# Kernel tuning notes

Hardware: AMD Instinct MI355X
Metric: run time of the kernel (lower is better)

The kernel has to match this reference:

```python
import jax, jax.numpy as jnp
import numpy as np
from jax import lax

B, C, H, W = 2, 128, 96, 96
K = 3
KK = K * K
EPS = 1e-5


def setup_inputs() -> dict:
    key = jax.random.key(0)
    ks = jax.random.split(key, 4)
    d = {"hu": jax.random.normal(ks[0], (B, C, H, W), jnp.float32)}
    for i in range(3):
        k = jax.random.split(ks[i + 1], 7)
        d["off_w%d" % (i + 1)] = jax.random.normal(k[0], (3 * KK, C, K, K), jnp.float32) * 0.01
        d["off_b%d" % (i + 1)] = jax.random.normal(k[1], (3 * KK,), jnp.float32) * 0.01
        d["w%d" % (i + 1)] = jax.random.normal(k[2], (C, C, K, K), jnp.float32) / np.float32(np.sqrt(C * KK))
        d["g%d" % (i + 1)] = jax.random.uniform(k[3], (C,), jnp.float32) + 0.5
        d["b%d" % (i + 1)] = jax.random.normal(k[4], (C,), jnp.float32) * 0.1
        d["m%d" % (i + 1)] = jax.random.normal(k[5], (C,), jnp.float32) * 0.1
        d["v%d" % (i + 1)] = jax.random.uniform(k[6], (C,), jnp.float32) + 0.5
    return d


def _mod_deform_conv(x, w, offset, mask, dilation):
    # x: [B,C,H,W]; offset: [B,2*KK,H,W] (dy,dx interleaved per kernel tap);
    # mask: [B,KK,H,W] (already sigmoid'ed). Zero padding outside the image.
    Hh, Ww = x.shape[2], x.shape[3]
    pad = dilation * (K - 1) // 2
    ky = jnp.repeat(jnp.arange(K), K).astype(x.dtype)  # [KK] row of each tap
    kx = jnp.tile(jnp.arange(K), K).astype(x.dtype)    # [KK] col of each tap
    gy = (jnp.arange(Hh, dtype=x.dtype) - pad)[None, :, None] + (ky * dilation)[:, None, None]  # [KK,H,1]
    gx = (jnp.arange(Ww, dtype=x.dtype) - pad)[None, None, :] + (kx * dilation)[:, None, None]  # [KK,1,W]
    off = offset.reshape(x.shape[0], KK, 2, Hh, Ww)
    py = gy[None] + off[:, :, 0]  # [B,KK,H,W] sampling row
    px = gx[None] + off[:, :, 1]  # [B,KK,H,W] sampling col

    def sample_one(xb, pyb, pxb, mb):
        # xb: [C,H,W]; pyb/pxb/mb: [KK,H,W]
        y0 = jnp.floor(pyb)
        x0 = jnp.floor(pxb)
        ly = pyb - y0
        lx = pxb - x0
        acc = jnp.zeros((xb.shape[0],) + pyb.shape, xb.dtype)
        for dy, wy in ((0, 1.0 - ly), (1, ly)):
            for dx, wx in ((0, 1.0 - lx), (1, lx)):
                yi = y0 + dy
                xi = x0 + dx
                valid = (yi >= 0) & (yi <= Hh - 1) & (xi >= 0) & (xi <= Ww - 1)
                yc = jnp.clip(yi, 0, Hh - 1).astype(jnp.int32)
                xc = jnp.clip(xi, 0, Ww - 1).astype(jnp.int32)
                v = xb[:, yc, xc]  # gather -> [C,KK,H,W]
                acc = acc + v * (wy * wx * valid.astype(xb.dtype))[None]
        return acc * mb[None]  # modulation

    sampled = jax.vmap(sample_one)(x, py, px, mask)  # [B,C,KK,H,W]
    return jnp.einsum('bckhw,ock->bohw', sampled, w.reshape(w.shape[0], w.shape[1], KK))


def _block(x, off_w, off_b, w, g, b, m, v, dilation):
    pad = dilation * (K - 1) // 2
    om = lax.conv_general_dilated(
        x, off_w, (1, 1), [(pad, pad), (pad, pad)],
        rhs_dilation=(dilation, dilation),
        dimension_numbers=('NCHW', 'OIHW', 'NCHW')) + off_b[None, :, None, None]
    offset = om[:, :2 * KK]
    mask = jax.nn.sigmoid(om[:, 2 * KK:])
    y = _mod_deform_conv(x, w, offset, mask, dilation)
    scale = (g / jnp.sqrt(v + EPS))[None, :, None, None]  # BN (inference form)
    y = (y - m[None, :, None, None]) * scale + b[None, :, None, None]
    return jax.nn.relu(y)


def reference(hu, off_w1, off_b1, w1, g1, b1, m1, v1,
              off_w2, off_b2, w2, g2, b2, m2, v2,
              off_w3, off_b3, w3, g3, b3, m3, v3):
    a1 = _block(hu, off_w1, off_b1, w1, g1, b1, m1, v1, 2) + hu
    a2 = _block(a1, off_w2, off_b2, w2, g2, b2, m2, v2, 4) + a1
    a3 = _block(a2, off_w3, off_b3, w3, g3, b3, m3, v3, 8) + a2
    return a3
```

## Files before the change

kernel.cpp:

```cpp
#include <hip/hip_runtime.h>
#include <math.h>

constexpr int Bn  = 2;
constexpr int Cn  = 128;
constexpr int Hn  = 96;
constexpr int Wn  = 96;
constexpr int HWn = Hn * Wn;
constexpr int CHWn = Cn * HWn;
constexpr int KCn = Cn * 9;
constexpr float EPSn = 1e-5f;
constexpr int KPAD = 1160;

typedef short bf16x8 __attribute__((ext_vector_type(8)));
typedef float f32x4  __attribute__((ext_vector_type(4)));

static __device__ inline short f2bf(float f) {
    union { float f; unsigned u; } v; v.f = f;
    unsigned r = v.u + 0x7fff + ((v.u >> 16) & 1);
    return (short)(r >> 16);
}
static __device__ inline unsigned pack2(float a, float b) {
    unsigned r;
    asm("v_cvt_pk_bf16_f32 %0, %1, %2" : "=v"(r) : "v"(a), "v"(b));
    return r;
}
static __device__ inline float bflo(unsigned u) { return __int_as_float(u << 16); }
static __device__ inline float bfhi(unsigned u) { return __int_as_float(u & 0xffff0000u); }

__global__ __launch_bounds__(256) void prep_all(
    const float* __restrict__ hu,
    const float* __restrict__ w1, const float* __restrict__ w2,
    const float* __restrict__ w3,
    const float* __restrict__ o1, const float* __restrict__ o2,
    const float* __restrict__ o3,
    short* __restrict__ wbs, short* __restrict__ owbs,
    unsigned short* __restrict__ xTb)
{
    __shared__ float Tl[128][65];
    const int bid = blockIdx.x;
    if (bid < 1728) {
        const int stage = bid / 576;
        const float* w = (stage == 0) ? w1 : (stage == 1) ? w2 : w3;
        int t = (bid - stage * 576) * 256 + threadIdx.x;
        int e = t & 7, l = (t >> 3) & 63, rest = t >> 9;
        int j = rest % 36, g = rest / 36;
        int lr = l & 15, lq = l >> 4;
        int o = g * 16 + lr;
        int kidx = j * 32 + lq * 8 + e;
        int k = kidx >> 7, c = kidx & 127;
        wbs[stage * Cn * KCn + t] = f2bf(w[o * KCn + c * 9 + k]);
    } else if (bid < 2160) {
        const int rb = bid - 1728;
        const int stage = rb / 144;
        const float* ow = (stage == 0) ? o1 : (stage == 1) ? o2 : o3;
        int t = (rb - stage * 144) * 256 + threadIdx.x;
        int e = t & 7, l = (t >> 3) & 63, rest = t >> 9;
        int kk = rest % 9, wvv = rest / 9;
        int mh = wvv & 1, ks = wvv >> 1;
        int lr = l & 15, lq = l >> 4;
        int o = mh * 16 + lr;
        int kidx = ks * 288 + kk * 32 + lq * 8 + e;
        int k = kidx >> 7, c = kidx & 127;
        owbs[stage * 32 * KCn + t] = (o < 27) ? f2bf(ow[o * KCn + c * 9 + k]) : (short)0;
    } else {
        const int t = threadIdx.x;
        const int pix0 = (bid - 2160) * 64;
        const int b   = pix0 / HWn;
        const int sp0 = pix0 - b * HWn;
        const float* xb = hu + b * CHWn + sp0 + (t & 63);
        const int c0 = t >> 6;
#pragma unroll 8
        for (int i = 0; i < 32; ++i) {
            const int c = c0 + 4 * i;
            Tl[c][t & 63] = xb[c * HWn];
        }
        __syncthreads();
        unsigned short* dstb = xTb + pix0 * 128;
#pragma unroll 8
        for (int i = 0; i < 32; ++i) {
            const int o = t + 256 * i;
            dstb[o] = (unsigned short)f2bf(Tl[o & 127][o >> 7]);
        }
    }
}

__global__ __launch_bounds__(512, 8) void fused_stage(
    const unsigned short* __restrict__ xTb,
    const short* __restrict__ wbs, const short* __restrict__ owbs,
    const float* __restrict__ obv,
    const float* __restrict__ gv, const float* __restrict__ bv,
    const float* __restrict__ mv, const float* __restrict__ vv,
    unsigned short* __restrict__ outTb,
    float* __restrict__ outC, int dil, int last)
{
    __shared__ short S[16 * KPAD];
    __shared__ float offL[16][18];
    __shared__ float maskL[16][9];

    const int t   = threadIdx.x;
    const int l   = t & 63;
    const int wv  = t >> 6;
    const int lh  = l >> 5;
    const int lc  = l & 31;

    const int bid = blockIdx.x;
    const int swz = (bid & 7) * 144 + (bid >> 3);
    const int pix0 = swz * 16;
    const int b   = pix0 / HWn;
    const int sp0 = pix0 - b * HWn;
    const int hy  = sp0 / Wn;
    const int wx0 = sp0 - hy * Wn;
    const int basep = b * HWn;

    bf16x8 oaf[6];
    {
        const short* oarow = owbs + (wv * 9) * 512 + l * 8;
#pragma unroll
        for (int u = 0; u < 6; ++u) oaf[u] = *(const bf16x8*)(oarow + u * 512);
    }

#pragma unroll
    for (int bch = 0; bch < 3; ++bch) {
        uint2 vle[3];
#pragma unroll
        for (int u = 0; u < 3; ++u) {
            const int k  = bch * 3 + u;
            const int pp = wv * 2 + lh;
            const int iy = hy + (k / 3 - 1) * dil;
            const int ix = wx0 + pp + (k % 3 - 1) * dil;
            const bool v = (iy >= 0) && (iy < Hn) && (ix >= 0) && (ix < Wn);
            const int aof = v ? (basep + iy * Wn + ix) : basep;
            uint2 val = ((const uint2*)(xTb + aof * 128))[lc];
            vle[u].x = v ? val.x : 0u;
            vle[u].y = v ? val.y : 0u;
        }
#pragma unroll
        for (int u = 0; u < 3; ++u) {
            const int k  = bch * 3 + u;
            const int pp = wv * 2 + lh;
            ((uint2*)&S[pp * KPAD + k * 128])[lc] = vle[u];
        }
    }
    __syncthreads();

    f32x4 oacc = {0.f, 0.f, 0.f, 0.f};
    {
        const int ks = wv >> 1;
        const short* oarow = owbs + (wv * 9) * 512 + l * 8;
        const short* srow  = &S[(l & 15) * KPAD + ks * 288 + ((l >> 4) * 8)];
#pragma unroll
        for (int bch = 0; bch < 2; ++bch) {
            bf16x8 bf[3];
#pragma unroll
            for (int u = 0; u < 3; ++u) bf[u] = *(const bf16x8*)(srow + (bch * 3 + u) * 32);
#pragma unroll
            for (int u = 0; u < 3; ++u)
                oacc = __builtin_amdgcn_mfma_f32_16x16x32_bf16(oaf[bch * 3 + u], bf[u], oacc, 0, 0, 0);
        }
        {
            bf16x8 af[3], bf[3];
#pragma unroll
            for (int u = 0; u < 3; ++u) af[u] = *(const bf16x8*)(oarow + (6 + u) * 512);
#pragma unroll
            for (int u = 0; u < 3; ++u) bf[u] = *(const bf16x8*)(srow + (6 + u) * 32);
#pragma unroll
            for (int u = 0; u < 3; ++u)
                oacc = __builtin_amdgcn_mfma_f32_16x16x32_bf16(af[u], bf[u], oacc, 0, 0, 0);
        }
    }
    __syncthreads();
    float* red = (float*)S;
    *(f32x4*)&red[wv * 256 + l * 4] = oacc;
    __syncthreads();
    if (wv < 2) {
        f32x4 s0 = *(const f32x4*)&red[(0 * 2 + wv) * 256 + l * 4];
        f32x4 s1 = *(const f32x4*)&red[(1 * 2 + wv) * 256 + l * 4];
        f32x4 s2 = *(const f32x4*)&red[(2 * 2 + wv) * 256 + l * 4];
        f32x4 s3 = *(const f32x4*)&red[(3 * 2 + wv) * 256 + l * 4];
        f32x4 sm = (s0 + s1) + (s2 + s3);
#pragma unroll
        for (int r = 0; r < 4; ++r) {
            int oc = wv * 16 + ((l >> 4) << 2) + r;
            if (oc < 18) {
                offL[l & 15][oc] = sm[r] + obv[oc];
            } else if (oc < 27) {
                float z = sm[r] + obv[oc];
                maskL[l & 15][oc - 18] = 1.f / (1.f + expf(-z));
            }
        }
    }
    __syncthreads();

    int pw0i = 0, pw1i = 0, pw2i = 0, pw3i = 0, pa0 = 0, pa1 = 0, pdx = 0;
    if (l < 18) {
        const int p = wv * 2 + l / 9;
        const int k = l - 9 * (l / 9);
        const float offy = offL[p][2 * k];
        const float offx = offL[p][2 * k + 1];
        const float m    = maskL[p][k];
        const float py = (float)(hy + (k / 3 - 1) * dil) + offy;
        const float px = (float)(wx0 + p + (k % 3 - 1) * dil) + offx;
        const float y0f = floorf(py), x0f = floorf(px);
        const float ly = py - y0f, lx = px - x0f;
        const int y0 = (int)y0f, x0 = (int)x0f;
        const float yv0 = (y0 >= 0 && y0 < Hn)      ? 1.f : 0.f;
        const float yv1 = (y0 >= -1 && y0 < Hn - 1) ? 1.f : 0.f;
        const float xv0 = (x0 >= 0 && x0 < Wn)      ? 1.f : 0.f;
        const float xv1 = (x0 >= -1 && x0 < Wn - 1) ? 1.f : 0.f;
        const float wy0 = (1.f - ly) * yv0 * m;
        const float wy1 = ly * yv1 * m;
        const float wxa = (1.f - lx) * xv0;
        const float wxb = lx * xv1;
        pw0i = __float_as_int(wy0 * wxa);
        pw1i = __float_as_int(wy0 * wxb);
        pw2i = __float_as_int(wy1 * wxa);
        pw3i = __float_as_int(wy1 * wxb);
        const int y0c = min(max(y0, 0), Hn - 1), y1c = min(max(y0 + 1, 0), Hn - 1);
        const int x0c = min(max(x0, 0), Wn - 1), x1c = min(max(x0 + 1, 0), Wn - 1);
        pa0 = (basep + y0c * Wn + x0c) * 128;
        pa1 = (basep + y1c * Wn + x1c) * 128;
        pdx = (x1c - x0c) * 128;
    }

    bf16x8 daf[4];
    {
        const short* darow = wbs + (wv * 36) * 512 + l * 8;
#pragma unroll
        for (int u = 0; u < 4; ++u) daf[u] = *(const bf16x8*)(darow + u * 512);
    }
    const int pp  = l & 15;
    const int ocb = wv * 16 + ((l >> 4) << 2);
    uint2 resb;
    if (last) {
        resb = *(const uint2*)&xTb[(pix0 + pp) * 128 + ocb];
    } else {
        const int o = t * 4;
        resb = *(const uint2*)&xTb[(pix0 + (o >> 7)) * 128 + (o & 127)];
    }

#pragma unroll
    for (int bch = 0; bch < 6; ++bch) {
        unsigned u00[3], u01[3], u10[3], u11[3];
        float    w00[3], w01[3], w10[3], w11[3];
#pragma unroll
        for (int u = 0; u < 3; ++u) {
            const int i = bch * 3 + u;
            w00[u] = __int_as_float(__builtin_amdgcn_readlane(pw0i, i));
            w01[u] = __int_as_float(__builtin_amdgcn_readlane(pw1i, i));
            w10[u] = __int_as_float(__builtin_amdgcn_readlane(pw2i, i));
            w11[u] = __int_as_float(__builtin_amdgcn_readlane(pw3i, i));
            const int a00 = __builtin_amdgcn_readlane(pa0, i);
            const int a11 = __builtin_amdgcn_readlane(pa1, i);
            const int dxk = __builtin_amdgcn_readlane(pdx, i);
            const unsigned short* xp = xTb + a00;
            const unsigned short* xq = xTb + a11;
            u00[u] = ((const unsigned*)xp)[l];
            u01[u] = ((const unsigned*)(xp + dxk))[l];
            u10[u] = ((const unsigned*)(xq - dxk))[l];
            u11[u] = ((const unsigned*)xq)[l];
        }
#pragma unroll
        for (int u = 0; u < 3; ++u) {
            const int i  = bch * 3 + u;
            const int di = i / 9;
            const int k  = i - di * 9;
            const int ppw = wv * 2 + di;
            float s0 = w00[u] * bflo(u00[u]) + w01[u] * bflo(u01[u])
                     + w10[u] * bflo(u10[u]) + w11[u] * bflo(u11[u]);
            float s1 = w00[u] * bfhi(u00[u]) + w01[u] * bfhi(u01[u])
                     + w10[u] * bfhi(u10[u]) + w11[u] * bfhi(u11[u]);
            ((unsigned*)&S[ppw * KPAD + k * 128])[l] = pack2(s0, s1);
        }
    }
    __syncthreads();

    f32x4 dacc = {0.f, 0.f, 0.f, 0.f};
    {
        const short* darow = wbs + (wv * 36) * 512 + l * 8;
        const short* srow  = &S[(l & 15) * KPAD + ((l >> 4) * 8)];
        {
            bf16x8 af45[2], bf[6];
            af45[0] = *(const bf16x8*)(darow + 4 * 512);
            af45[1] = *(const bf16x8*)(darow + 5 * 512);
#pragma unroll
            for (int u = 0; u < 6; ++u) bf[u] = *(const bf16x8*)(srow + u * 32);
#pragma unroll
            for (int u = 0; u < 4; ++u)
                dacc = __builtin_amdgcn_mfma_f32_16x16x32_bf16(daf[u], bf[u], dacc, 0, 0, 0);
            dacc = __builtin_amdgcn_mfma_f32_16x16x32_bf16(af45[0], bf[4], dacc, 0, 0, 0);
            dacc = __builtin_amdgcn_mfma_f32_16x16x32_bf16(af45[1], bf[5], dacc, 0, 0, 0);
        }
#pragma unroll
        for (int bch = 1; bch < 6; ++bch) {
            bf16x8 af[6], bf[6];
#pragma unroll
            for (int u = 0; u < 6; ++u) af[u] = *(const bf16x8*)(darow + (bch * 6 + u) * 512);
#pragma unroll
            for (int u = 0; u < 6; ++u) bf[u] = *(const bf16x8*)(srow  + (bch * 6 + u) * 32);
#pragma unroll
            for (int u = 0; u < 6; ++u)
                dacc = __builtin_amdgcn_mfma_f32_16x16x32_bf16(af[u], bf[u], dacc, 0, 0, 0);
        }
    }

    if (last) {
        const float rs[4] = {bflo(resb.x), bfhi(resb.x), bflo(resb.y), bfhi(resb.y)};
#pragma unroll
        for (int r = 0; r < 4; ++r) {
            const int oc = ocb + r;
            const float sc = gv[oc] * rsqrtf(vv[oc] + EPSn);
            float y = (dacc[r] - mv[oc]) * sc + bv[oc];
            y = fmaxf(y, 0.f) + rs[r];
            outC[b * CHWn + oc * HWn + sp0 + pp] = y;
        }
    } else {
        __syncthreads();
        float* O = (float*)S;
#pragma unroll
        for (int r = 0; r < 4; ++r) {
            const int oc = ocb + r;
            const float sc = gv[oc] * rsqrtf(vv[oc] + EPSn);
            float y = (dacc[r] - mv[oc]) * sc + bv[oc];
            O[pp * 132 + oc] = fmaxf(y, 0.f);
        }
        __syncthreads();
        const int o  = t * 4;
        const int qp = o >> 7, qc = o & 127;
        f32x4 yv = *(f32x4*)&O[qp * 132 + qc];
        yv[0] += bflo(resb.x);
        yv[1] += bfhi(resb.x);
        yv[2] += bflo(resb.y);
        yv[3] += bfhi(resb.y);
        uint2 pk;
        pk.x = pack2(yv[0], yv[1]);
        pk.y = pack2(yv[2], yv[3]);
        *(uint2*)&outTb[(pix0 + qp) * 128 + qc] = pk;
    }
}

extern "C" void kernel_launch(void* const* d_in, const int* in_sizes, int n_in,
                              void* d_out, int out_size, void* d_ws, size_t ws_size,
                              hipStream_t stream) {
    (void)in_sizes; (void)n_in; (void)out_size; (void)ws_size;

    const float* hu = (const float*)d_in[0];

    short* wbs  = (short*)d_ws;
    short* owbs = wbs + 3 * Cn * KCn;
    unsigned short* T0b = (unsigned short*)(owbs + 3 * 32 * KCn);
    unsigned short* T1b = T0b + Bn * CHWn;

    prep_all<<<2448, 256, 0, stream>>>(
        hu,
        (const float*)d_in[3], (const float*)d_in[10], (const float*)d_in[17],
        (const float*)d_in[1], (const float*)d_in[8], (const float*)d_in[15],
        wbs, owbs, T0b);

    const int dils[3] = {2, 4, 8};
    const unsigned short* insb[3] = {T0b, T1b, T0b};
    unsigned short* outsb[3] = {T1b, T0b, nullptr};
    const int nblk = (Bn * HWn) / 16;

    for (int i = 0; i < 3; ++i) {
        const float* obv = (const float*)d_in[2 + 7 * i];
        const float* gv  = (const float*)d_in[4 + 7 * i];
        const float* bv  = (const float*)d_in[5 + 7 * i];
        const float* mv  = (const float*)d_in[6 + 7 * i];
        const float* vv  = (const float*)d_in[7 + 7 * i];
        const int last = (i == 2);

        fused_stage<<<nblk, 512, 0, stream>>>(
            insb[i], wbs + i * Cn * KCn, owbs + i * 32 * KCn, obv,
            gv, bv, mv, vv, outsb[i],
            last ? (float*)d_out : nullptr, dils[i], last);
    }
}
```

Baseline: 100.7 us.

## Overlap next-stage weight reshuffle with current fused stage via extra blocks

The prep kernel now converts only stage 1 weights and the input transpose. Conversion of the next stage's conv and offset weights to bf16 is done by extra blocks appended to each fused_stage launch, which return early after their conversion work. The aim is to shorten the serial prep kernel and hide the weight shuffle behind the compute of the previous stage. The extra 512-thread blocks compete for CU slots and may delay tail blocks of the main work.

```diff
diff --git a/kernel.cpp b/kernel.cpp
--- a/kernel.cpp
+++ b/kernel.cpp
@@ -27,44 +27,45 @@
 static __device__ inline float bflo(unsigned u) { return __int_as_float(u << 16); }
 static __device__ inline float bfhi(unsigned u) { return __int_as_float(u & 0xffff0000u); }
 
-__global__ __launch_bounds__(256) void prep_all(
+static __device__ inline void shuf_w(int t, const float* __restrict__ w,
+                                     short* __restrict__ dst)
+{
+    int e = t & 7, l = (t >> 3) & 63, rest = t >> 9;
+    int j = rest % 36, g = rest / 36;
+    int lr = l & 15, lq = l >> 4;
+    int o = g * 16 + lr;
+    int kidx = j * 32 + lq * 8 + e;
+    int k = kidx >> 7, c = kidx & 127;
+    dst[t] = f2bf(w[o * KCn + c * 9 + k]);
+}
+static __device__ inline void shuf_ow(int t, const float* __restrict__ ow,
+                                      short* __restrict__ dst)
+{
+    int e = t & 7, l = (t >> 3) & 63, rest = t >> 9;
+    int kk = rest % 9, wvv = rest / 9;
+    int mh = wvv & 1, ks = wvv >> 1;
+    int lr = l & 15, lq = l >> 4;
+    int o = mh * 16 + lr;
+    int kidx = ks * 288 + kk * 32 + lq * 8 + e;
+    int k = kidx >> 7, c = kidx & 127;
+    dst[t] = (o < 27) ? f2bf(ow[o * KCn + c * 9 + k]) : (short)0;
+}
+
+__global__ __launch_bounds__(256) void prep_s1(
     const float* __restrict__ hu,
-    const float* __restrict__ w1, const float* __restrict__ w2,
-    const float* __restrict__ w3,
-    const float* __restrict__ o1, const float* __restrict__ o2,
-    const float* __restrict__ o3,
+    const float* __restrict__ w1, const float* __restrict__ o1,
     short* __restrict__ wbs, short* __restrict__ owbs,
     unsigned short* __restrict__ xTb)
 {
     __shared__ float Tl[128][65];
     const int bid = blockIdx.x;
-    if (bid < 1728) {
-        const int stage = bid / 576;
-        const float* w = (stage == 0) ? w1 : (stage == 1) ? w2 : w3;
-        int t = (bid - stage * 576) * 256 + threadIdx.x;
-        int e = t & 7, l = (t >> 3) & 63, rest = t >> 9;
-        int j = rest % 36, g = rest / 36;
-        int lr = l & 15, lq = l >> 4;
-        int o = g * 16 + lr;
-        int kidx = j * 32 + lq * 8 + e;
-        int k = kidx >> 7, c = kidx & 127;
-        wbs[stage * Cn * KCn + t] = f2bf(w[o * KCn + c * 9 + k]);
-    } else if (bid < 2160) {
-        const int rb = bid - 1728;
-        const int stage = rb / 144;
-        const float* ow = (stage == 0) ? o1 : (stage == 1) ? o2 : o3;
-        int t = (rb - stage * 144) * 256 + threadIdx.x;
-        int e = t & 7, l = (t >> 3) & 63, rest = t >> 9;
-        int kk = rest % 9, wvv = rest / 9;
-        int mh = wvv & 1, ks = wvv >> 1;
-        int lr = l & 15, lq = l >> 4;
-        int o = mh * 16 + lr;
-        int kidx = ks * 288 + kk * 32 + lq * 8 + e;
-        int k = kidx >> 7, c = kidx & 127;
-        owbs[stage * 32 * KCn + t] = (o < 27) ? f2bf(ow[o * KCn + c * 9 + k]) : (short)0;
+    if (bid < 576) {
+        shuf_w(bid * 256 + threadIdx.x, w1, wbs);
+    } else if (bid < 720) {
+        shuf_ow((bid - 576) * 256 + threadIdx.x, o1, owbs);
     } else {
         const int t = threadIdx.x;
-        const int pix0 = (bid - 2160) * 64;
+        const int pix0 = (bid - 720) * 64;
         const int b   = pix0 / HWn;
         const int sp0 = pix0 - b * HWn;
         const float* xb = hu + b * CHWn + sp0 + (t & 63);
@@ -91,11 +92,24 @@
     const float* __restrict__ gv, const float* __restrict__ bv,
     const float* __restrict__ mv, const float* __restrict__ vv,
     unsigned short* __restrict__ outTb,
-    float* __restrict__ outC, int dil, int last)
+    float* __restrict__ outC, int dil, int last,
+    const float* __restrict__ wnext, const float* __restrict__ ownext,
+    short* __restrict__ wbs_next, short* __restrict__ owbs_next)
 {
     __shared__ short S[16 * KPAD];
     __shared__ float offL[16][18];
     __shared__ float maskL[16][9];
+
+    const int bid = blockIdx.x;
+    if (bid >= 1152) {
+        const int rb = bid - 1152;
+        if (rb < 288) {
+            shuf_w(rb * 512 + threadIdx.x, wnext, wbs_next);
+        } else {
+            shuf_ow((rb - 288) * 512 + threadIdx.x, ownext, owbs_next);
+        }
+        return;
+    }
 
     const int t   = threadIdx.x;
     const int l   = t & 63;
@@ -103,7 +117,6 @@
     const int lh  = l >> 5;
     const int lc  = l & 31;
 
-    const int bid = blockIdx.x;
     const int swz = (bid & 7) * 144 + (bid >> 3);
     const int pix0 = swz * 16;
     const int b   = pix0 / HWn;
@@ -350,16 +363,12 @@
     unsigned short* T0b = (unsigned short*)(owbs + 3 * 32 * KCn);
     unsigned short* T1b = T0b + Bn * CHWn;
 
-    prep_all<<<2448, 256, 0, stream>>>(
-        hu,
-        (const float*)d_in[3], (const float*)d_in[10], (const float*)d_in[17],
-        (const float*)d_in[1], (const float*)d_in[8], (const float*)d_in[15],
-        wbs, owbs, T0b);
+    prep_s1<<<1008, 256, 0, stream>>>(
+        hu, (const float*)d_in[3], (const float*)d_in[1], wbs, owbs, T0b);
 
     const int dils[3] = {2, 4, 8};
     const unsigned short* insb[3] = {T0b, T1b, T0b};
     unsigned short* outsb[3] = {T1b, T0b, nullptr};
-    const int nblk = (Bn * HWn) / 16;
 
     for (int i = 0; i < 3; ++i) {
         const float* obv = (const float*)d_in[2 + 7 * i];
@@ -369,9 +378,16 @@
         const float* vv  = (const float*)d_in[7 + 7 * i];
         const int last = (i == 2);
 
+        const int nblk = last ? 1152 : 1152 + 360;
+        const float* wnext  = last ? nullptr : (const float*)d_in[3 + 7 * (i + 1)];
+        const float* ownext = last ? nullptr : (const float*)d_in[1 + 7 * (i + 1)];
+        short* wbs_next  = last ? nullptr : wbs  + (i + 1) * Cn * KCn;
+        short* owbs_next = last ? nullptr : owbs + (i + 1) * 32 * KCn;
+
         fused_stage<<<nblk, 512, 0, stream>>>(
             insb[i], wbs + i * Cn * KCn, owbs + i * 32 * KCn, obv,
             gv, bv, mv, vv, outsb[i],
-            last ? (float*)d_out : nullptr, dils[i], last);
-    }
-}
+            last ? (float*)d_out : nullptr, dils[i], last,
+            wnext, ownext, wbs_next, owbs_next);
+    }
+}
```

Result: faster. 98.64 us (-2.0%).
